# Kernel optimization log

Hardware: AMD Instinct MI355X
Metric: run time of the kernel (lower is better)

## Reference

```python
import jax, jax.numpy as jnp
import numpy as np
from jax import lax

T, B, V, N = 128, 256, 256, 1024


def setup_inputs() -> dict:
    key = jax.random.key(0)
    k1, k2, k3, k4 = jax.random.split(key, 4)
    inputs = jax.random.uniform(k1, (T, B, V), dtype=jnp.float32)
    labels = jax.random.uniform(k2, (T * B, V), dtype=jnp.float32)
    weights = jax.random.normal(k3, (V + N, N), dtype=jnp.float32) * 0.1
    bias = jnp.zeros((N,), dtype=jnp.float32)
    output_weights = jax.random.normal(k4, (N, V), dtype=jnp.float32) * 0.1
    output_bias = jnp.zeros((V,), dtype=jnp.float32)
    return {
        "inputs": inputs,
        "labels": labels,
        "weights": weights,
        "bias": bias,
        "output_weights": output_weights,
        "output_bias": output_bias,
    }


def reference(inputs, labels, weights, bias, output_weights, output_bias):
    t, b, v = inputs.shape
    n = weights.shape[1]
    # split concat-matmul into x@Wx + h@Wh (same math as concat([x,h]) @ W)
    w_x = weights[:v]   # [V, N]
    w_h = weights[v:]   # [N, N]

    def step(h, x):
        h_new = jnp.tanh(x @ w_x + h @ w_h + bias)
        return h_new, h_new

    h0 = jnp.zeros((b, n), dtype=inputs.dtype)
    _, outputs = lax.scan(step, h0, inputs)          # [T, B, N]
    outputs = outputs.reshape(t * b, n)              # concat over time
    logits = outputs @ output_weights + output_bias  # [T*B, V]
    # softmax_cross_entropy_with_logits (soft labels), then mean
    log_p = jax.nn.log_softmax(logits, axis=-1)
    loss = jnp.mean(-jnp.sum(labels * log_p, axis=-1))
    return loss
```

## Files before the change

kernel.cpp:

```cpp
#include <hip/hip_runtime.h>
#include <math.h>

typedef __bf16 bf16;
typedef __attribute__((ext_vector_type(4))) __bf16 bf16x4;
typedef __attribute__((ext_vector_type(8))) __bf16 bf16x8;
typedef __attribute__((ext_vector_type(4))) float f32x4;

#define T_STEPS 128
#define B_SZ    256
#define V_SZ    256
#define N_SZ    1024
#define NROWS   (T_STEPS * B_SZ)
#define RSTR    68
#define LSTR    17
#define NGRP    16
#define NCB     16

__device__ __forceinline__ float fast_tanh(float x) {
    float e = __expf(2.0f * x);
    return 1.0f - 2.0f / (e + 1.0f);
}

__device__ __forceinline__ bf16x8 cvt_bf16x8(float4 a, float4 b) {
    bf16x8 r;
    r[0] = (bf16)a.x; r[1] = (bf16)a.y; r[2] = (bf16)a.z; r[3] = (bf16)a.w;
    r[4] = (bf16)b.x; r[5] = (bf16)b.y; r[6] = (bf16)b.z; r[7] = (bf16)b.w;
    return r;
}

__global__ __launch_bounds__(256) void k_prep(
    const float* __restrict__ weights,
    const float* __restrict__ out_w,
    bf16* __restrict__ Wxt,
    bf16* __restrict__ Wht,
    bf16* __restrict__ Wot)
{
    __shared__ float tile[32][33];
    int id = blockIdx.x;
    const float* src; bf16* dst; int R, C, tr, tc;
    if (id < 256) {
        src = weights; dst = Wxt; R = V_SZ; C = N_SZ;
        tr = (id & 7) * 32; tc = (id >> 3) * 32;
    } else if (id < 1280) {
        id -= 256;
        src = weights + (size_t)V_SZ * N_SZ; dst = Wht; R = N_SZ; C = N_SZ;
        tr = (id & 31) * 32; tc = (id >> 5) * 32;
    } else {
        id -= 1280;
        src = out_w; dst = Wot; R = N_SZ; C = V_SZ;
        tr = (id & 31) * 32; tc = (id >> 5) * 32;
    }
    int tx = threadIdx.x & 31;
    int ty = threadIdx.x >> 5;
#pragma unroll
    for (int i = 0; i < 32; i += 8)
        tile[ty + i][tx] = src[(size_t)(tr + ty + i) * C + tc + tx];
    __syncthreads();
#pragma unroll
    for (int i = 0; i < 32; i += 8)
        dst[(size_t)(tc + ty + i) * R + tr + tx] = (bf16)tile[tx][ty + i];
}

__global__ __launch_bounds__(512, 2) void k_rnn(
    const float* __restrict__ Xf,
    const bf16* __restrict__ Wxt,
    const bf16* __restrict__ Wht,
    const bf16* __restrict__ Wot,
    const float* __restrict__ bias,
    bf16* __restrict__ XH,
    unsigned int* __restrict__ Lgu,
    int* __restrict__ cnt)
{
    __shared__ float red[8 * 16 * RSTR];
    __shared__ float lred[8 * 16 * LSTR];
    const int tid  = threadIdx.x;
    const int lane = tid & 63;
    const int w    = tid >> 6;
    const int quad = lane >> 4;
    const int l15  = lane & 15;
    const int g  = blockIdx.x >> 4;
    const int c  = blockIdx.x & 15;
    const int m0 = g * 16;
    const int n0 = c * 64;
    const int k0 = w * 128;
    const int v0 = w * 32;
    int* gcnt = cnt + g * T_STEPS;

    const bf16* Bp = Wht + (size_t)(n0 + l15) * N_SZ + k0 + quad * 8;
    bf16x8 b[4][4];
#pragma unroll
    for (int nt = 0; nt < 4; ++nt)
#pragma unroll
        for (int kc = 0; kc < 4; ++kc)
            b[nt][kc] = *(const bf16x8*)&Bp[(size_t)(nt * 16) * N_SZ + kc * 32];
    bf16x8 bx[4];
#pragma unroll
    for (int nt = 0; nt < 4; ++nt)
        bx[nt] = *(const bf16x8*)&Wxt[(size_t)(n0 + nt * 16 + l15) * V_SZ + v0 + quad * 8];
    bf16x8 bo[4];
#pragma unroll
    for (int kc = 0; kc < 4; ++kc)
        bo[kc] = *(const bf16x8*)&Wot[(size_t)(c * 16 + l15) * N_SZ + k0 + kc * 32 + quad * 8];

    const int orow = tid >> 5;
    const int ocol = (tid & 31) * 2;
    const float bias0 = bias[n0 + ocol];
    const float bias1 = bias[n0 + ocol + 1];
    const int lrow = w * 2 + (lane >> 3);
    const int lvp  = lane & 7;
    unsigned int* XHu = (unsigned int*)XH;
    const f32x4 zz = {0.f, 0.f, 0.f, 0.f};
    const size_t xin = (size_t)(m0 + l15) * V_SZ + v0 + quad * 8;

    {
        float4 f0 = *(const float4*)&Xf[xin];
        float4 f1 = *(const float4*)&Xf[xin + 4];
        bf16x8 ax = cvt_bf16x8(f0, f1);
        f32x4 acc[4] = {zz, zz, zz, zz};
#pragma unroll
        for (int nt = 0; nt < 4; ++nt)
            acc[nt] = __builtin_amdgcn_mfma_f32_16x16x32_bf16(ax, bx[nt], acc[nt], 0, 0, 0);
#pragma unroll
        for (int nt = 0; nt < 4; ++nt)
#pragma unroll
            for (int r = 0; r < 4; ++r)
                red[(w * 16 + quad * 4 + r) * RSTR + nt * 16 + l15] = acc[nt][r];
        __syncthreads();
        float s0 = bias0, s1 = bias1;
#pragma unroll
        for (int w2 = 0; w2 < 8; ++w2) {
            float2 v = *(const float2*)&red[(w2 * 16 + orow) * RSTR + ocol];
            s0 += v.x; s1 += v.y;
        }
        bf16 r0 = (bf16)fast_tanh(s0);
        bf16 r1 = (bf16)fast_tanh(s1);
        unsigned int outw = (unsigned int)__builtin_bit_cast(unsigned short, r0)
                          | ((unsigned int)__builtin_bit_cast(unsigned short, r1) << 16);
        size_t oidx = (((size_t)m0 + orow) * N_SZ + n0 + ocol) >> 1;
        __hip_atomic_store(&XHu[oidx], outw, __ATOMIC_RELAXED, __HIP_MEMORY_SCOPE_AGENT);
        asm volatile("s_waitcnt vmcnt(0)" ::: "memory");
        __syncthreads();
        if (tid == 0)
            __hip_atomic_fetch_add(&gcnt[0], 1, __ATOMIC_RELAXED, __HIP_MEMORY_SCOPE_AGENT);
    }

    for (int t = 1; t < T_STEPS; ++t) {
        float4 f0 = *(const float4*)&Xf[(size_t)t * B_SZ * V_SZ + xin];
        float4 f1 = *(const float4*)&Xf[(size_t)t * B_SZ * V_SZ + xin + 4];
        int cv = __hip_atomic_load(&gcnt[t - 1], __ATOMIC_RELAXED,
                                   __HIP_MEMORY_SCOPE_AGENT);

        bf16x8 ax = cvt_bf16x8(f0, f1);
        f32x4 acc[4] = {zz, zz, zz, zz};
#pragma unroll
        for (int nt = 0; nt < 4; ++nt)
            acc[nt] = __builtin_amdgcn_mfma_f32_16x16x32_bf16(ax, bx[nt], acc[nt], 0, 0, 0);
        asm volatile("" : "+v"(acc[0]), "+v"(acc[1]), "+v"(acc[2]), "+v"(acc[3]));

        while (cv < NCB) {
            __builtin_amdgcn_s_sleep(1);
            cv = __hip_atomic_load(&gcnt[t - 1], __ATOMIC_RELAXED,
                                   __HIP_MEMORY_SCOPE_AGENT);
        }
        asm volatile("" ::: "memory");

        const bf16* Ap = XH + ((size_t)(t - 1) * B_SZ + m0 + l15) * N_SZ + k0 + quad * 8;
        bf16x8 a[4];
#pragma unroll
        for (int kc = 0; kc < 4; ++kc)
            a[kc] = *(const bf16x8*)&Ap[kc * 32];

#pragma unroll
        for (int kc = 0; kc < 4; ++kc)
#pragma unroll
            for (int nt = 0; nt < 4; ++nt)
                acc[nt] = __builtin_amdgcn_mfma_f32_16x16x32_bf16(a[kc], b[nt][kc],
                                                                  acc[nt], 0, 0, 0);
        f32x4 lacc = zz;
#pragma unroll
        for (int kc = 0; kc < 4; ++kc)
            lacc = __builtin_amdgcn_mfma_f32_16x16x32_bf16(a[kc], bo[kc], lacc, 0, 0, 0);

#pragma unroll
        for (int nt = 0; nt < 4; ++nt)
#pragma unroll
            for (int r = 0; r < 4; ++r)
                red[(w * 16 + quad * 4 + r) * RSTR + nt * 16 + l15] = acc[nt][r];
#pragma unroll
        for (int r = 0; r < 4; ++r)
            lred[(w * 16 + quad * 4 + r) * LSTR + l15] = lacc[r];
        __syncthreads();

        float s0 = bias0, s1 = bias1;
#pragma unroll
        for (int w2 = 0; w2 < 8; ++w2) {
            float2 v = *(const float2*)&red[(w2 * 16 + orow) * RSTR + ocol];
            s0 += v.x; s1 += v.y;
        }
        bf16 r0 = (bf16)fast_tanh(s0);
        bf16 r1 = (bf16)fast_tanh(s1);
        unsigned int outw = (unsigned int)__builtin_bit_cast(unsigned short, r0)
                          | ((unsigned int)__builtin_bit_cast(unsigned short, r1) << 16);
        size_t oidx = (((size_t)t * B_SZ + m0 + orow) * N_SZ + n0 + ocol) >> 1;
        __hip_atomic_store(&XHu[oidx], outw, __ATOMIC_RELAXED, __HIP_MEMORY_SCOPE_AGENT);
        asm volatile("" ::: "memory");

        if (lane < 16) {
            float sa = 0.f, sb = 0.f;
#pragma unroll
            for (int w2 = 0; w2 < 8; ++w2) {
                sa += lred[(w2 * 16 + lrow) * LSTR + lvp * 2];
                sb += lred[(w2 * 16 + lrow) * LSTR + lvp * 2 + 1];
            }
            bf16 pa = (bf16)sa, pb = (bf16)sb;
            unsigned int pw = (unsigned int)__builtin_bit_cast(unsigned short, pa)
                            | ((unsigned int)__builtin_bit_cast(unsigned short, pb) << 16);
            Lgu[(((size_t)(t - 1) * 16 + c) * B_SZ + m0 + lrow) * 8 + lvp] = pw;
        }

        asm volatile("s_waitcnt vmcnt(1)" ::: "memory");
        __syncthreads();
        if (tid == 0)
            __hip_atomic_fetch_add(&gcnt[t], 1, __ATOMIC_RELAXED, __HIP_MEMORY_SCOPE_AGENT);
    }

    {
        int cv = __hip_atomic_load(&gcnt[T_STEPS - 1], __ATOMIC_RELAXED,
                                   __HIP_MEMORY_SCOPE_AGENT);
        while (cv < NCB) {
            __builtin_amdgcn_s_sleep(1);
            cv = __hip_atomic_load(&gcnt[T_STEPS - 1], __ATOMIC_RELAXED,
                                   __HIP_MEMORY_SCOPE_AGENT);
        }
        asm volatile("" ::: "memory");
        const bf16* Ap = XH + ((size_t)(T_STEPS - 1) * B_SZ + m0 + l15) * N_SZ + k0 + quad * 8;
        bf16x8 a[4];
#pragma unroll
        for (int kc = 0; kc < 4; ++kc)
            a[kc] = *(const bf16x8*)&Ap[kc * 32];
        f32x4 lacc = zz;
#pragma unroll
        for (int kc = 0; kc < 4; ++kc)
            lacc = __builtin_amdgcn_mfma_f32_16x16x32_bf16(a[kc], bo[kc], lacc, 0, 0, 0);
#pragma unroll
        for (int r = 0; r < 4; ++r)
            lred[(w * 16 + quad * 4 + r) * LSTR + l15] = lacc[r];
        __syncthreads();
        if (lane < 16) {
            float sa = 0.f, sb = 0.f;
#pragma unroll
            for (int w2 = 0; w2 < 8; ++w2) {
                sa += lred[(w2 * 16 + lrow) * LSTR + lvp * 2];
                sb += lred[(w2 * 16 + lrow) * LSTR + lvp * 2 + 1];
            }
            bf16 pa = (bf16)sa, pb = (bf16)sb;
            unsigned int pw = (unsigned int)__builtin_bit_cast(unsigned short, pa)
                            | ((unsigned int)__builtin_bit_cast(unsigned short, pb) << 16);
            Lgu[(((size_t)(T_STEPS - 1) * 16 + c) * B_SZ + m0 + lrow) * 8 + lvp] = pw;
        }
    }
}

__global__ __launch_bounds__(512) void k_lred(
    const bf16* __restrict__ Lg,
    const float* __restrict__ labels,
    const float* __restrict__ ob,
    float* __restrict__ out)
{
    __shared__ float bt[8];
    const int tid  = threadIdx.x;
    const int lane = tid & 63;
    const int w    = tid >> 6;
    const int cs   = lane >> 2;
    const int vi   = (lane & 3) * 4;
    const float4 ob4 = *(const float4*)&ob[cs * 16 + vi];

    float wtot = 0.f;
#pragma unroll
    for (int i = 0; i < 8; ++i) {
        int row  = blockIdx.x * 64 + w * 8 + i;
        int p    = row >> 8;
        int brow = row & 255;
        bf16x4 lv = *(const bf16x4*)&Lg[(((size_t)p * 16 + cs) * B_SZ + brow) * 16 + vi];
        float l0 = (float)lv.x + ob4.x;
        float l1 = (float)lv.y + ob4.y;
        float l2 = (float)lv.z + ob4.z;
        float l3 = (float)lv.w + ob4.w;
        float mx = fmaxf(fmaxf(l0, l1), fmaxf(l2, l3));
#pragma unroll
        for (int sft = 1; sft < 64; sft <<= 1)
            mx = fmaxf(mx, __shfl_xor(mx, sft, 64));
        float sume = __expf(l0 - mx) + __expf(l1 - mx) + __expf(l2 - mx) + __expf(l3 - mx);
        const float4 lb = *(const float4*)&labels[(size_t)row * V_SZ + cs * 16 + vi];
        float labs = lb.x + lb.y + lb.z + lb.w;
        float labv = lb.x * l0 + lb.y * l1 + lb.z * l2 + lb.w * l3;
#pragma unroll
        for (int sft = 1; sft < 64; sft <<= 1) {
            sume += __shfl_xor(sume, sft, 64);
            labs += __shfl_xor(labs, sft, 64);
            labv += __shfl_xor(labv, sft, 64);
        }
        float lse = mx + __logf(sume);
        wtot += labs * lse - labv;
    }
    if (lane == 0) bt[w] = wtot;
    __syncthreads();
    if (tid == 0) {
        float s = bt[0] + bt[1] + bt[2] + bt[3] + bt[4] + bt[5] + bt[6] + bt[7];
        atomicAdd(out, s * (1.0f / (float)NROWS));
    }
}

extern "C" void kernel_launch(void* const* d_in, const int* in_sizes, int n_in,
                              void* d_out, int out_size, void* d_ws, size_t ws_size,
                              hipStream_t stream)
{
    const float* inputs  = (const float*)d_in[0];
    const float* labels  = (const float*)d_in[1];
    const float* weights = (const float*)d_in[2];
    const float* bias    = (const float*)d_in[3];
    const float* out_w   = (const float*)d_in[4];
    const float* out_b   = (const float*)d_in[5];
    float* out = (float*)d_out;

    char* ws = (char*)d_ws;
    bf16* XH  = (bf16*)ws;  ws += (size_t)NROWS * N_SZ * 2;
    bf16* Lg  = (bf16*)ws;  ws += (size_t)NROWS * V_SZ * 2;
    bf16* Wxt = (bf16*)ws;  ws += (size_t)N_SZ * V_SZ * 2;
    bf16* Wht = (bf16*)ws;  ws += (size_t)N_SZ * N_SZ * 2;
    bf16* Wot = (bf16*)ws;  ws += (size_t)V_SZ * N_SZ * 2;
    int*  cnt = (int*)ws;   ws += (size_t)NGRP * T_STEPS * 4;

    hipMemsetAsync(out, 0, sizeof(float), stream);
    hipMemsetAsync(cnt, 0, (size_t)NGRP * T_STEPS * 4, stream);

    k_prep<<<dim3(1536), 256, 0, stream>>>(weights, out_w, Wxt, Wht, Wot);

    k_rnn<<<dim3(NGRP * NCB), 512, 0, stream>>>(inputs, Wxt, Wht, Wot, bias, XH,
                                                (unsigned int*)Lg, cnt);

    k_lred<<<dim3(NROWS / 64), 512, 0, stream>>>(Lg, labels, out_b, out);
}
```

Before: 474.8 us.

## Replace per-step atomic counter with per-block flags and signal earlier

Each block now writes its own completion flag per timestep instead of atomically incrementing a shared counter, and waiters poll all 16 flags in parallel across lanes, checking them with a wave vote. The flag is published right after the hidden state store, before the logits partial reduction, so dependent blocks can start sooner. The logits reduction scratch is double-buffered by timestep parity so the earlier barrier does not race with the next step's writes. This shortens the critical path of the cross-block recurrence at the cost of a larger flag array.

```diff
diff --git a/kernel.cpp b/kernel.cpp
--- a/kernel.cpp
+++ b/kernel.cpp
@@ -69,10 +69,10 @@
     const float* __restrict__ bias,
     bf16* __restrict__ XH,
     unsigned int* __restrict__ Lgu,
-    int* __restrict__ cnt)
+    int* __restrict__ flg)
 {
     __shared__ float red[8 * 16 * RSTR];
-    __shared__ float lred[8 * 16 * LSTR];
+    __shared__ float lred[2][8 * 16 * LSTR];
     const int tid  = threadIdx.x;
     const int lane = tid & 63;
     const int w    = tid >> 6;
@@ -84,7 +84,7 @@
     const int n0 = c * 64;
     const int k0 = w * 128;
     const int v0 = w * 32;
-    int* gcnt = cnt + g * T_STEPS;
+    int* gflg = flg + g * (T_STEPS * 16);
 
     const bf16* Bp = Wht + (size_t)(n0 + l15) * N_SZ + k0 + quad * 8;
     bf16x8 b[4][4];
@@ -141,14 +141,15 @@
         asm volatile("s_waitcnt vmcnt(0)" ::: "memory");
         __syncthreads();
         if (tid == 0)
-            __hip_atomic_fetch_add(&gcnt[0], 1, __ATOMIC_RELAXED, __HIP_MEMORY_SCOPE_AGENT);
+            __hip_atomic_store(&gflg[0 * 16 + c], 1, __ATOMIC_RELAXED,
+                               __HIP_MEMORY_SCOPE_AGENT);
     }
 
     for (int t = 1; t < T_STEPS; ++t) {
         float4 f0 = *(const float4*)&Xf[(size_t)t * B_SZ * V_SZ + xin];
         float4 f1 = *(const float4*)&Xf[(size_t)t * B_SZ * V_SZ + xin + 4];
-        int cv = __hip_atomic_load(&gcnt[t - 1], __ATOMIC_RELAXED,
-                                   __HIP_MEMORY_SCOPE_AGENT);
+        const int* fpp = gflg + (t - 1) * 16 + l15;
+        int fv = __hip_atomic_load(fpp, __ATOMIC_RELAXED, __HIP_MEMORY_SCOPE_AGENT);
 
         bf16x8 ax = cvt_bf16x8(f0, f1);
         f32x4 acc[4] = {zz, zz, zz, zz};
@@ -157,10 +158,9 @@
             acc[nt] = __builtin_amdgcn_mfma_f32_16x16x32_bf16(ax, bx[nt], acc[nt], 0, 0, 0);
         asm volatile("" : "+v"(acc[0]), "+v"(acc[1]), "+v"(acc[2]), "+v"(acc[3]));
 
-        while (cv < NCB) {
+        while (!__all(fv != 0)) {
             __builtin_amdgcn_s_sleep(1);
-            cv = __hip_atomic_load(&gcnt[t - 1], __ATOMIC_RELAXED,
-                                   __HIP_MEMORY_SCOPE_AGENT);
+            fv = __hip_atomic_load(fpp, __ATOMIC_RELAXED, __HIP_MEMORY_SCOPE_AGENT);
         }
         asm volatile("" ::: "memory");
 
@@ -188,7 +188,7 @@
                 red[(w * 16 + quad * 4 + r) * RSTR + nt * 16 + l15] = acc[nt][r];
 #pragma unroll
         for (int r = 0; r < 4; ++r)
-            lred[(w * 16 + quad * 4 + r) * LSTR + l15] = lacc[r];
+            lred[t & 1][(w * 16 + quad * 4 + r) * LSTR + l15] = lacc[r];
         __syncthreads();
 
         float s0 = bias0, s1 = bias1;
@@ -203,34 +203,33 @@
                           | ((unsigned int)__builtin_bit_cast(unsigned short, r1) << 16);
         size_t oidx = (((size_t)t * B_SZ + m0 + orow) * N_SZ + n0 + ocol) >> 1;
         __hip_atomic_store(&XHu[oidx], outw, __ATOMIC_RELAXED, __HIP_MEMORY_SCOPE_AGENT);
-        asm volatile("" ::: "memory");
+
+        asm volatile("s_waitcnt vmcnt(0)" ::: "memory");
+        __syncthreads();
+        if (tid == 0)
+            __hip_atomic_store(&gflg[t * 16 + c], 1, __ATOMIC_RELAXED,
+                               __HIP_MEMORY_SCOPE_AGENT);
 
         if (lane < 16) {
             float sa = 0.f, sb = 0.f;
 #pragma unroll
             for (int w2 = 0; w2 < 8; ++w2) {
-                sa += lred[(w2 * 16 + lrow) * LSTR + lvp * 2];
-                sb += lred[(w2 * 16 + lrow) * LSTR + lvp * 2 + 1];
+                sa += lred[t & 1][(w2 * 16 + lrow) * LSTR + lvp * 2];
+                sb += lred[t & 1][(w2 * 16 + lrow) * LSTR + lvp * 2 + 1];
             }
             bf16 pa = (bf16)sa, pb = (bf16)sb;
             unsigned int pw = (unsigned int)__builtin_bit_cast(unsigned short, pa)
                             | ((unsigned int)__builtin_bit_cast(unsigned short, pb) << 16);
             Lgu[(((size_t)(t - 1) * 16 + c) * B_SZ + m0 + lrow) * 8 + lvp] = pw;
         }
-
-        asm volatile("s_waitcnt vmcnt(1)" ::: "memory");
-        __syncthreads();
-        if (tid == 0)
-            __hip_atomic_fetch_add(&gcnt[t], 1, __ATOMIC_RELAXED, __HIP_MEMORY_SCOPE_AGENT);
     }
 
     {
-        int cv = __hip_atomic_load(&gcnt[T_STEPS - 1], __ATOMIC_RELAXED,
-                                   __HIP_MEMORY_SCOPE_AGENT);
-        while (cv < NCB) {
+        const int* fpp = gflg + (T_STEPS - 1) * 16 + l15;
+        int fv = __hip_atomic_load(fpp, __ATOMIC_RELAXED, __HIP_MEMORY_SCOPE_AGENT);
+        while (!__all(fv != 0)) {
             __builtin_amdgcn_s_sleep(1);
-            cv = __hip_atomic_load(&gcnt[T_STEPS - 1], __ATOMIC_RELAXED,
-                                   __HIP_MEMORY_SCOPE_AGENT);
+            fv = __hip_atomic_load(fpp, __ATOMIC_RELAXED, __HIP_MEMORY_SCOPE_AGENT);
         }
         asm volatile("" ::: "memory");
         const bf16* Ap = XH + ((size_t)(T_STEPS - 1) * B_SZ + m0 + l15) * N_SZ + k0 + quad * 8;
@@ -244,14 +243,14 @@
             lacc = __builtin_amdgcn_mfma_f32_16x16x32_bf16(a[kc], bo[kc], lacc, 0, 0, 0);
 #pragma unroll
         for (int r = 0; r < 4; ++r)
-            lred[(w * 16 + quad * 4 + r) * LSTR + l15] = lacc[r];
+            lred[0][(w * 16 + quad * 4 + r) * LSTR + l15] = lacc[r];
         __syncthreads();
         if (lane < 16) {
             float sa = 0.f, sb = 0.f;
 #pragma unroll
             for (int w2 = 0; w2 < 8; ++w2) {
-                sa += lred[(w2 * 16 + lrow) * LSTR + lvp * 2];
-                sb += lred[(w2 * 16 + lrow) * LSTR + lvp * 2 + 1];
+                sa += lred[0][(w2 * 16 + lrow) * LSTR + lvp * 2];
+                sb += lred[0][(w2 * 16 + lrow) * LSTR + lvp * 2 + 1];
             }
             bf16 pa = (bf16)sa, pb = (bf16)sb;
             unsigned int pw = (unsigned int)__builtin_bit_cast(unsigned short, pa)
@@ -329,15 +328,15 @@
     bf16* Wxt = (bf16*)ws;  ws += (size_t)N_SZ * V_SZ * 2;
     bf16* Wht = (bf16*)ws;  ws += (size_t)N_SZ * N_SZ * 2;
     bf16* Wot = (bf16*)ws;  ws += (size_t)V_SZ * N_SZ * 2;
-    int*  cnt = (int*)ws;   ws += (size_t)NGRP * T_STEPS * 4;
+    int*  flg = (int*)ws;   ws += (size_t)NGRP * T_STEPS * 16 * 4;
 
     hipMemsetAsync(out, 0, sizeof(float), stream);
-    hipMemsetAsync(cnt, 0, (size_t)NGRP * T_STEPS * 4, stream);
+    hipMemsetAsync(flg, 0, (size_t)NGRP * T_STEPS * 16 * 4, stream);
 
     k_prep<<<dim3(1536), 256, 0, stream>>>(weights, out_w, Wxt, Wht, Wot);
 
     k_rnn<<<dim3(NGRP * NCB), 512, 0, stream>>>(inputs, Wxt, Wht, Wot, bias, XH,
-                                                (unsigned int*)Lg, cnt);
+                                                (unsigned int*)Lg, flg);
 
     k_lred<<<dim3(NROWS / 64), 512, 0, stream>>>(Lg, labels, out_b, out);
 }
```

Result: slower. 509.5 us (+7.3%).

## Overlap loss reduction with RNN recurrence and fold memsets into prep kernel

Applied to the files above, without the earlier changes.

Removes the separate loss kernel and instead launches 64 extra blocks inside the RNN kernel. Each extra block spins on per-group step counters and reduces the cross-entropy for two timesteps as soon as their logits are published. The counter and output zeroing moves into an extra block of the prep kernel, replacing two memset calls. This hides the loss pass behind the sequential recurrence. In exchange the counters now require a full vmcnt(0) wait before each increment, and the spinning blocks take CU slots and memory bandwidth away from the recurrence blocks, which could deadlock if they are scheduled first and the recurrence blocks cannot become resident.

```diff
diff --git a/kernel.cpp b/kernel.cpp
--- a/kernel.cpp
+++ b/kernel.cpp
@@ -7,6 +7,7 @@
 typedef __attribute__((ext_vector_type(4))) float f32x4;
 
 #define T_STEPS 128
+#define TS1     (T_STEPS + 1)
 #define B_SZ    256
 #define V_SZ    256
 #define N_SZ    1024
@@ -15,6 +16,7 @@
 #define LSTR    17
 #define NGRP    16
 #define NCB     16
+#define NLOSS   64
 
 __device__ __forceinline__ float fast_tanh(float x) {
     float e = __expf(2.0f * x);
@@ -33,10 +35,17 @@
     const float* __restrict__ out_w,
     bf16* __restrict__ Wxt,
     bf16* __restrict__ Wht,
-    bf16* __restrict__ Wot)
+    bf16* __restrict__ Wot,
+    int*  __restrict__ cnt,
+    float* __restrict__ out)
 {
     __shared__ float tile[32][33];
     int id = blockIdx.x;
+    if (id == 1536) {
+        for (int i = threadIdx.x; i < NGRP * TS1; i += 256) cnt[i] = 0;
+        if (threadIdx.x == 0) out[0] = 0.f;
+        return;
+    }
     const float* src; bf16* dst; int R, C, tr, tc;
     if (id < 256) {
         src = weights; dst = Wxt; R = V_SZ; C = N_SZ;
@@ -69,22 +78,81 @@
     const float* __restrict__ bias,
     bf16* __restrict__ XH,
     unsigned int* __restrict__ Lgu,
-    int* __restrict__ cnt)
+    int* __restrict__ cnt,
+    const float* __restrict__ labels,
+    const float* __restrict__ ob,
+    float* __restrict__ out)
 {
     __shared__ float red[8 * 16 * RSTR];
     __shared__ float lred[8 * 16 * LSTR];
+    __shared__ float bt[8];
     const int tid  = threadIdx.x;
     const int lane = tid & 63;
     const int w    = tid >> 6;
     const int quad = lane >> 4;
     const int l15  = lane & 15;
+
+    if (blockIdx.x >= NGRP * NCB) {
+        const int lb = blockIdx.x - NGRP * NCB;
+        const bf16* Lg = (const bf16*)Lgu;
+        const int cs = lane >> 2;
+        const int vi = (lane & 3) * 4;
+        const float4 ob4 = *(const float4*)&ob[cs * 16 + vi];
+        float wtot = 0.f;
+#pragma unroll
+        for (int pp = 0; pp < 2; ++pp) {
+            const int p = lb * 2 + pp;
+            const int* cp = cnt + (lane & 15) * TS1 + (p + 1);
+            int v = (lane < 16) ? __hip_atomic_load(cp, __ATOMIC_RELAXED,
+                                                    __HIP_MEMORY_SCOPE_AGENT) : NCB;
+            while (!__all(v >= NCB)) {
+                __builtin_amdgcn_s_sleep(32);
+                v = (lane < 16) ? __hip_atomic_load(cp, __ATOMIC_RELAXED,
+                                                    __HIP_MEMORY_SCOPE_AGENT) : NCB;
+            }
+            asm volatile("" ::: "memory");
+            for (int i = 0; i < 32; ++i) {
+                int brow = w * 32 + i;
+                bf16x4 lv = *(const bf16x4*)&Lg[(((size_t)p * 16 + cs) * B_SZ + brow) * 16 + vi];
+                float l0 = (float)lv.x + ob4.x;
+                float l1 = (float)lv.y + ob4.y;
+                float l2 = (float)lv.z + ob4.z;
+                float l3 = (float)lv.w + ob4.w;
+                float mx = fmaxf(fmaxf(l0, l1), fmaxf(l2, l3));
+#pragma unroll
+                for (int sft = 1; sft < 64; sft <<= 1)
+                    mx = fmaxf(mx, __shfl_xor(mx, sft, 64));
+                float sume = __expf(l0 - mx) + __expf(l1 - mx)
+                           + __expf(l2 - mx) + __expf(l3 - mx);
+                const float4 lb4 = *(const float4*)
+                    &labels[((size_t)p * B_SZ + brow) * V_SZ + cs * 16 + vi];
+                float labs = lb4.x + lb4.y + lb4.z + lb4.w;
+                float labv = lb4.x * l0 + lb4.y * l1 + lb4.z * l2 + lb4.w * l3;
+#pragma unroll
+                for (int sft = 1; sft < 64; sft <<= 1) {
+                    sume += __shfl_xor(sume, sft, 64);
+                    labs += __shfl_xor(labs, sft, 64);
+                    labv += __shfl_xor(labv, sft, 64);
+                }
+                wtot += labs * (mx + __logf(sume)) - labv;
+            }
+        }
+        if (lane == 0) bt[w] = wtot;
+        __syncthreads();
+        if (tid == 0) {
+            float s = bt[0] + bt[1] + bt[2] + bt[3] + bt[4] + bt[5] + bt[6] + bt[7];
+            atomicAdd(out, s * (1.0f / (float)NROWS));
+        }
+        return;
+    }
+
     const int g  = blockIdx.x >> 4;
     const int c  = blockIdx.x & 15;
     const int m0 = g * 16;
     const int n0 = c * 64;
     const int k0 = w * 128;
     const int v0 = w * 32;
-    int* gcnt = cnt + g * T_STEPS;
+    int* gcnt = cnt + g * TS1;
 
     const bf16* Bp = Wht + (size_t)(n0 + l15) * N_SZ + k0 + quad * 8;
     bf16x8 b[4][4];
@@ -203,7 +271,6 @@
                           | ((unsigned int)__builtin_bit_cast(unsigned short, r1) << 16);
         size_t oidx = (((size_t)t * B_SZ + m0 + orow) * N_SZ + n0 + ocol) >> 1;
         __hip_atomic_store(&XHu[oidx], outw, __ATOMIC_RELAXED, __HIP_MEMORY_SCOPE_AGENT);
-        asm volatile("" ::: "memory");
 
         if (lane < 16) {
             float sa = 0.f, sb = 0.f;
@@ -218,7 +285,7 @@
             Lgu[(((size_t)(t - 1) * 16 + c) * B_SZ + m0 + lrow) * 8 + lvp] = pw;
         }
 
-        asm volatile("s_waitcnt vmcnt(1)" ::: "memory");
+        asm volatile("s_waitcnt vmcnt(0)" ::: "memory");
         __syncthreads();
         if (tid == 0)
             __hip_atomic_fetch_add(&gcnt[t], 1, __ATOMIC_RELAXED, __HIP_MEMORY_SCOPE_AGENT);
@@ -258,56 +325,11 @@
                             | ((unsigned int)__builtin_bit_cast(unsigned short, pb) << 16);
             Lgu[(((size_t)(T_STEPS - 1) * 16 + c) * B_SZ + m0 + lrow) * 8 + lvp] = pw;
         }
-    }
-}
-
-__global__ __launch_bounds__(512) void k_lred(
-    const bf16* __restrict__ Lg,
-    const float* __restrict__ labels,
-    const float* __restrict__ ob,
-    float* __restrict__ out)
-{
-    __shared__ float bt[8];
-    const int tid  = threadIdx.x;
-    const int lane = tid & 63;
-    const int w    = tid >> 6;
-    const int cs   = lane >> 2;
-    const int vi   = (lane & 3) * 4;
-    const float4 ob4 = *(const float4*)&ob[cs * 16 + vi];
-
-    float wtot = 0.f;
-#pragma unroll
-    for (int i = 0; i < 8; ++i) {
-        int row  = blockIdx.x * 64 + w * 8 + i;
-        int p    = row >> 8;
-        int brow = row & 255;
-        bf16x4 lv = *(const bf16x4*)&Lg[(((size_t)p * 16 + cs) * B_SZ + brow) * 16 + vi];
-        float l0 = (float)lv.x + ob4.x;
-        float l1 = (float)lv.y + ob4.y;
-        float l2 = (float)lv.z + ob4.z;
-        float l3 = (float)lv.w + ob4.w;
-        float mx = fmaxf(fmaxf(l0, l1), fmaxf(l2, l3));
-#pragma unroll
-        for (int sft = 1; sft < 64; sft <<= 1)
-            mx = fmaxf(mx, __shfl_xor(mx, sft, 64));
-        float sume = __expf(l0 - mx) + __expf(l1 - mx) + __expf(l2 - mx) + __expf(l3 - mx);
-        const float4 lb = *(const float4*)&labels[(size_t)row * V_SZ + cs * 16 + vi];
-        float labs = lb.x + lb.y + lb.z + lb.w;
-        float labv = lb.x * l0 + lb.y * l1 + lb.z * l2 + lb.w * l3;
-#pragma unroll
-        for (int sft = 1; sft < 64; sft <<= 1) {
-            sume += __shfl_xor(sume, sft, 64);
-            labs += __shfl_xor(labs, sft, 64);
-            labv += __shfl_xor(labv, sft, 64);
-        }
-        float lse = mx + __logf(sume);
-        wtot += labs * lse - labv;
-    }
-    if (lane == 0) bt[w] = wtot;
-    __syncthreads();
-    if (tid == 0) {
-        float s = bt[0] + bt[1] + bt[2] + bt[3] + bt[4] + bt[5] + bt[6] + bt[7];
-        atomicAdd(out, s * (1.0f / (float)NROWS));
+        asm volatile("s_waitcnt vmcnt(0)" ::: "memory");
+        __syncthreads();
+        if (tid == 0)
+            __hip_atomic_fetch_add(&gcnt[T_STEPS], 1, __ATOMIC_RELAXED,
+                                   __HIP_MEMORY_SCOPE_AGENT);
     }
 }
 
@@ -329,15 +351,11 @@
     bf16* Wxt = (bf16*)ws;  ws += (size_t)N_SZ * V_SZ * 2;
     bf16* Wht = (bf16*)ws;  ws += (size_t)N_SZ * N_SZ * 2;
     bf16* Wot = (bf16*)ws;  ws += (size_t)V_SZ * N_SZ * 2;
-    int*  cnt = (int*)ws;   ws += (size_t)NGRP * T_STEPS * 4;
-
-    hipMemsetAsync(out, 0, sizeof(float), stream);
-    hipMemsetAsync(cnt, 0, (size_t)NGRP * T_STEPS * 4, stream);
-
-    k_prep<<<dim3(1536), 256, 0, stream>>>(weights, out_w, Wxt, Wht, Wot);
-
-    k_rnn<<<dim3(NGRP * NCB), 512, 0, stream>>>(inputs, Wxt, Wht, Wot, bias, XH,
-                                                (unsigned int*)Lg, cnt);
-
-    k_lred<<<dim3(NROWS / 64), 512, 0, stream>>>(Lg, labels, out_b, out);
-}
+    int*  cnt = (int*)ws;   ws += (size_t)NGRP * TS1 * 4;
+
+    k_prep<<<dim3(1537), 256, 0, stream>>>(weights, out_w, Wxt, Wht, Wot, cnt, out);
+
+    k_rnn<<<dim3(NGRP * NCB + NLOSS), 512, 0, stream>>>(inputs, Wxt, Wht, Wot, bias,
+                                                        XH, (unsigned int*)Lg, cnt,
+                                                        labels, out_b, out);
+}
```

Result: slower. 528.8 us (+11.4%).
